# Performance work log

Hardware: AMD Instinct MI355X
Metric: run time of the kernel (lower is better)

The kernel has to match this reference:

```python
import jax, jax.numpy as jnp
import numpy as np

B, S, D, H = 4, 2048, 1024, 16
HD = D // H
BITS = 8
LEVELS = 2 ** BITS - 1          # number of negative log2 levels
SCALING = 32.0 / 16.0           # lora alpha / rank for 8-bit adapter
NEG_INF = -1e9


def log_fake_quant(x, reduce_axes):
    """Per-channel log-domain fake quantization with straight-through estimator.
    Scale = per-channel max-abs; magnitudes snapped to power-of-two fractions of scale."""
    s = jnp.maximum(jnp.max(jnp.abs(x), axis=reduce_axes, keepdims=True), 1e-8)
    ratio = jnp.clip(jnp.abs(x) / s, 2.0 ** (-LEVELS), 1.0)
    e = jnp.round(jnp.log2(ratio))                      # in [-LEVELS, 0]
    q = jnp.sign(x) * s * jnp.exp2(e)
    return x + jax.lax.stop_gradient(q - x)             # STE


def cpt_linear(x, W, b, lA, lB):
    """CPTLinear: fake-quantized activation/weight GEMM + bias + LoRA on the fp input."""
    xq = log_fake_quant(x, tuple(range(x.ndim - 1)))     # per last-dim channel
    Wq = log_fake_quant(W, (1,))                         # per output row (channel_dim=0)
    out = xq @ Wq.T + b
    return out + (x @ lA @ lB) * SCALING


def setup_inputs() -> dict:
    key = jax.random.key(0)
    ks = jax.random.split(key, 8)
    causal = jnp.tril(jnp.ones((S, S), dtype=bool))
    mask = jnp.where(causal, 0.0, NEG_INF).astype(jnp.float32)[None, None]  # [1,1,S,S]
    return {
        "hidden_states": jax.random.normal(ks[0], (B, S, D), jnp.float32),
        "attention_mask": mask,
        "W_attn": jax.random.normal(ks[1], (3 * D, D), jnp.float32) * 0.02,
        "b_attn": jnp.zeros((3 * D,), jnp.float32),
        "lA_attn": jax.random.normal(ks[2], (D, 16), jnp.float32) * 0.01,
        "lB_attn": jax.random.normal(ks[3], (16, 3 * D), jnp.float32) * 0.01,
        "W_proj": jax.random.normal(ks[4], (D, D), jnp.float32) * 0.02,
        "b_proj": jnp.zeros((D,), jnp.float32),
        "lA_proj": jax.random.normal(ks[5], (D, 16), jnp.float32) * 0.01,
        "lB_proj": jax.random.normal(ks[6], (16, D), jnp.float32) * 0.01,
    }


def reference(hidden_states, attention_mask, W_attn, b_attn, lA_attn, lB_attn,
              W_proj, b_proj, lA_proj, lB_proj):
    qkv = cpt_linear(hidden_states, W_attn, b_attn, lA_attn, lB_attn)  # [B,S,3D]
    q, k, v = jnp.split(qkv, 3, axis=-1)

    def to_heads(t):
        return t.reshape(B, S, H, HD).transpose(0, 2, 1, 3)            # [B,H,S,HD]

    q, k, v = to_heads(q), to_heads(k), to_heads(v)
    scores = jnp.einsum("bhqd,bhkd->bhqk", q, k) / np.float32(np.sqrt(HD))
    scores = scores + attention_mask
    attn = jax.nn.softmax(scores, axis=-1)                             # dropout: eval mode (identity)
    out = jnp.einsum("bhqk,bhkd->bhqd", attn, v)
    out = out.transpose(0, 2, 1, 3).reshape(B, S, D)
    return cpt_linear(out, W_proj, b_proj, lA_proj, lB_proj)
```

## Files before the change

kernel.cpp:

```cpp
#include <hip/hip_runtime.h>

#define SS 2048
#define DD 1024
#define DQKV 3072
#define KP 1088
#define NT64 17
#define MTOT 8192
#define QKSZ ((size_t)MTOT * DD)
#define SCL 0.18033688011112042f

typedef unsigned short us;
typedef __attribute__((ext_vector_type(8))) short bf16x8;
typedef __attribute__((ext_vector_type(4))) float f32x4;
typedef __attribute__((ext_vector_type(4))) unsigned u32x4;

#define WAITVM(N) asm volatile("s_waitcnt vmcnt(" #N ")" ::: "memory")
#define WAITLGKM0 asm volatile("s_waitcnt lgkmcnt(0)" ::: "memory")

__device__ __forceinline__ us f2bf(float f) {
    unsigned u = __float_as_uint(f);
    return (us)((u + 0x7fffu + ((u >> 16) & 1u)) >> 16);
}
__device__ __forceinline__ float bf2f(us h) { return __uint_as_float(((unsigned)h) << 16); }
__device__ __forceinline__ void split2(float q, us& h, us& l) {
    h = f2bf(q); l = f2bf(q - bf2f(h));
}
__device__ __forceinline__ unsigned cvtpk(float lo, float hi) {
    unsigned r;
    asm("v_cvt_pk_bf16_f32 %0, %1, %2" : "=v"(r) : "v"(lo), "v"(hi));
    return r;
}

__device__ __forceinline__ int logq_e(float ax, float s) {
    int e = 0;
    if (ax < s) {
        double r = (double)ax / (double)s;
        int ex;
        double mant = frexp(r, &ex);
        e = (mant >= 0.70710678118654752440) ? ex : ex - 1;
        e = (e < -255) ? -255 : e;
    }
    return e;
}
__device__ __forceinline__ float logq_exact(float x, float s) {
    float ax = fabsf(x);
    if (ax == 0.f) return copysignf(0.f, x);
    return copysignf(ldexpf(s, logq_e(ax, s)), x);
}

__device__ __forceinline__ void gll16(const void* g, void* l) {
    __builtin_amdgcn_global_load_lds(
        (const __attribute__((address_space(1))) void*)g,
        (__attribute__((address_space(3))) void*)l, 16, 0, 0);
}


__global__ void k_zero(unsigned* p, int n) {
    int i = blockIdx.x * 256 + threadIdx.x;
    if (i < n) p[i] = 0u;
}

__global__ void k_colmax(const float* __restrict__ x, unsigned* __restrict__ smax) {
    int c = blockIdx.x * 256 + threadIdx.x;
    int r0 = blockIdx.y * 128;
    float m = 0.f;
    for (int r = 0; r < 128; ++r) m = fmaxf(m, fabsf(x[(size_t)(r0 + r) * DD + c]));
    atomicMax(smax + c, __float_as_uint(m));
}

__global__ __launch_bounds__(256) void k_quant_lora(const float* __restrict__ x,
                                                    const unsigned* __restrict__ smax,
                                                    const float* __restrict__ lA,
                                                    us* __restrict__ xq) {
    __shared__ float red[4][16];
    int m = blockIdx.x, tx = threadIdx.x;
    int lane = tx & 63, w = tx >> 6;
    float4 xv = ((const float4*)(x + (size_t)m * DD))[tx];
    int c = tx * 4;
    float vv[4] = {xv.x, xv.y, xv.z, xv.w};
    ushort4 qh;
    us* ph = (us*)&qh;
#pragma unroll
    for (int j = 0; j < 4; ++j) {
        float s = fmaxf(__uint_as_float(smax[c + j]), 1e-8f);
        float sh = bf2f(f2bf(s));
        float ax = fabsf(vv[j]);
        if (ax == 0.f) ph[j] = (us)((__float_as_uint(vv[j]) >> 16) & 0x8000u);
        else ph[j] = f2bf(copysignf(ldexpf(sh, logq_e(ax, s)), vv[j]));
    }
    *(ushort4*)(xq + (size_t)m * KP + c) = qh;
    float acc[16];
#pragma unroll
    for (int r = 0; r < 16; ++r) acc[r] = 0.f;
#pragma unroll
    for (int j = 0; j < 4; ++j) {
        float xs = vv[j];
        const float4* lr = (const float4*)(lA + (size_t)(c + j) * 16);
        float4 a0 = lr[0], a1 = lr[1], a2 = lr[2], a3 = lr[3];
        acc[0] += xs * a0.x; acc[1] += xs * a0.y; acc[2] += xs * a0.z; acc[3] += xs * a0.w;
        acc[4] += xs * a1.x; acc[5] += xs * a1.y; acc[6] += xs * a1.z; acc[7] += xs * a1.w;
        acc[8] += xs * a2.x; acc[9] += xs * a2.y; acc[10] += xs * a2.z; acc[11] += xs * a2.w;
        acc[12] += xs * a3.x; acc[13] += xs * a3.y; acc[14] += xs * a3.z; acc[15] += xs * a3.w;
    }
#pragma unroll
    for (int msk = 1; msk < 64; msk <<= 1)
#pragma unroll
        for (int r = 0; r < 16; ++r) acc[r] += __shfl_xor(acc[r], msk);
    if (lane == 0)
#pragma unroll
        for (int r = 0; r < 16; ++r) red[w][r] = acc[r];
    __syncthreads();
    if (tx < 16) {
        float v = 2.0f * (red[0][tx] + red[1][tx] + red[2][tx] + red[3][tx]);
        us h, l; split2(v, h, l);
        xq[(size_t)m * KP + 1024 + tx] = h;
        xq[(size_t)m * KP + 1040 + tx] = l;
    } else if (tx == 16) {
        xq[(size_t)m * KP + 1056] = 0x3F80;
    } else if (tx < 48) {
        xq[(size_t)m * KP + 1040 + tx] = 0;
    }
}

__global__ __launch_bounds__(256) void k_quant_w(const float* __restrict__ W, const float* __restrict__ lB,
                                                 const float* __restrict__ bias,
                                                 const unsigned* __restrict__ smax,
                                                 us* __restrict__ wh, us* __restrict__ wl, int Nn) {
    __shared__ float red[4];
    int n = blockIdx.x, tx = threadIdx.x;
    int lane = tx & 63, w = tx >> 6;
    float4 wv = ((const float4*)(W + (size_t)n * DD))[tx];
    float m4 = fmaxf(fmaxf(fabsf(wv.x), fabsf(wv.y)), fmaxf(fabsf(wv.z), fabsf(wv.w)));
#pragma unroll
    for (int msk = 1; msk < 64; msk <<= 1) m4 = fmaxf(m4, __shfl_xor(m4, msk));
    if (lane == 0) red[w] = m4;
    __syncthreads();
    float t = fmaxf(fmaxf(fmaxf(red[0], red[1]), fmaxf(red[2], red[3])), 1e-8f);
    float vv[4] = {wv.x, wv.y, wv.z, wv.w};
    int c = tx * 4;
    ushort4 qh, ql;
    us* ph = (us*)&qh; us* pl = (us*)&ql;
#pragma unroll
    for (int j = 0; j < 4; ++j) {
        float s = fmaxf(__uint_as_float(smax[c + j]), 1e-8f);
        float sh = bf2f(f2bf(s));
        float rho = (s - sh) / sh;
        float q = logq_exact(vv[j], t);
        float wp = q + q * rho;
        split2(wp, ph[j], pl[j]);
    }
    *(ushort4*)(wh + (size_t)n * KP + c) = qh;
    *(ushort4*)(wl + (size_t)n * KP + c) = ql;
    if (tx < 64) {
        us h = 0, l = 0;
        if (tx < 32) { int r = tx & 15; split2(lB[(size_t)r * Nn + n], h, l); }
        else if (tx == 32) split2(bias[n], h, l);
        wh[(size_t)n * KP + 1024 + tx] = h;
        wl[(size_t)n * KP + 1024 + tx] = l;
    }
}


template <int MODE>
__global__ __launch_bounds__(512, 2) void k_gemm(const us* __restrict__ Aq_,
                                                 const us* __restrict__ Bh_, const us* __restrict__ Bl_,
                                                 float* __restrict__ C, int Nn,
                                                 us* __restrict__ Khg, us* __restrict__ Klg,
                                                 float* __restrict__ vbuf) {
    __shared__ us LA[2][16384];
    __shared__ us LBh[2][8192];
    __shared__ us LBl[2][8192];
    int tid = threadIdx.x;
    int bm = blockIdx.x, bn = blockIdx.y;
    int lane = tid & 63, w = tid >> 6;
    int wm = w >> 2, wn = w & 3;
    int l15 = lane & 15, l4 = lane >> 4;
    int srow = tid >> 3;
    int gsrc = ((tid & 7) ^ (srow & 7)) * 8;
    const us* aP  = Aq_ + (size_t)(bm * 256 + srow) * KP + gsrc;
    const us* bhP = Bh_ + (size_t)(bn * 128 + srow) * KP + gsrc;
    const us* blP = Bl_ + (size_t)(bn * 128 + srow) * KP + gsrc;
    f32x4 zero4 = {0.f, 0.f, 0.f, 0.f};
    f32x4 acc[8][2];
#pragma unroll
    for (int i = 0; i < 8; ++i) { acc[i][0] = zero4; acc[i][1] = zero4; }

#define GSTAGE(buf, kt)                                               \
    do {                                                              \
        int k0_ = (kt) * 64;                                          \
        gll16(aP + k0_,                    &LA[(buf)][0]     + tid * 8); \
        gll16(aP + (size_t)64  * KP + k0_, &LA[(buf)][4096]  + tid * 8); \
        gll16(aP + (size_t)128 * KP + k0_, &LA[(buf)][8192]  + tid * 8); \
        gll16(aP + (size_t)192 * KP + k0_, &LA[(buf)][12288] + tid * 8); \
        gll16(bhP + k0_,                   &LBh[(buf)][0]    + tid * 8); \
        gll16(bhP + (size_t)64 * KP + k0_, &LBh[(buf)][4096] + tid * 8); \
        gll16(blP + k0_,                   &LBl[(buf)][0]    + tid * 8); \
        gll16(blP + (size_t)64 * KP + k0_, &LBl[(buf)][4096] + tid * 8); \
    } while (0)

    GSTAGE(0, 0);
    GSTAGE(1, 1);
    WAITVM(8);
    __builtin_amdgcn_s_barrier();
    __builtin_amdgcn_sched_barrier(0);

    int gsw0 = ((l4)     ^ (l15 & 7)) * 8;
    int gsw1 = ((4 + l4) ^ (l15 & 7)) * 8;
    int cur = 0;
    for (int kt = 0; kt < NT64; ++kt) {
        const us* A0  = &LA[cur][0];
        const us* Bh0 = &LBh[cur][0];
        const us* Bl0 = &LBl[cur][0];
        bf16x8 a0[8], b0h[2], b0l[2];
#pragma unroll
        for (int i = 0; i < 8; ++i)
            a0[i] = *(const bf16x8*)(A0 + (wm * 128 + i * 16 + l15) * 64 + gsw0);
#pragma unroll
        for (int i = 0; i < 2; ++i) {
            b0h[i] = *(const bf16x8*)(Bh0 + (wn * 32 + i * 16 + l15) * 64 + gsw0);
            b0l[i] = *(const bf16x8*)(Bl0 + (wn * 32 + i * 16 + l15) * 64 + gsw0);
        }
        __builtin_amdgcn_s_setprio(1);
#pragma unroll
        for (int mi = 0; mi < 8; ++mi)
#pragma unroll
            for (int ni = 0; ni < 2; ++ni) {
                acc[mi][ni] = __builtin_amdgcn_mfma_f32_16x16x32_bf16(a0[mi], b0h[ni], acc[mi][ni], 0, 0, 0);
                acc[mi][ni] = __builtin_amdgcn_mfma_f32_16x16x32_bf16(a0[mi], b0l[ni], acc[mi][ni], 0, 0, 0);
            }
        __builtin_amdgcn_s_setprio(0);
        bf16x8 a1[8], b1h[2], b1l[2];
#pragma unroll
        for (int i = 0; i < 8; ++i)
            a1[i] = *(const bf16x8*)(A0 + (wm * 128 + i * 16 + l15) * 64 + gsw1);
#pragma unroll
        for (int i = 0; i < 2; ++i) {
            b1h[i] = *(const bf16x8*)(Bh0 + (wn * 32 + i * 16 + l15) * 64 + gsw1);
            b1l[i] = *(const bf16x8*)(Bl0 + (wn * 32 + i * 16 + l15) * 64 + gsw1);
        }
        WAITLGKM0;
        __builtin_amdgcn_sched_barrier(0);
        __builtin_amdgcn_s_barrier();
        __builtin_amdgcn_sched_barrier(0);
        if (kt + 2 < NT64) GSTAGE(cur, kt + 2);
        __builtin_amdgcn_s_setprio(1);
#pragma unroll
        for (int mi = 0; mi < 8; ++mi)
#pragma unroll
            for (int ni = 0; ni < 2; ++ni) {
                acc[mi][ni] = __builtin_amdgcn_mfma_f32_16x16x32_bf16(a1[mi], b1h[ni], acc[mi][ni], 0, 0, 0);
                acc[mi][ni] = __builtin_amdgcn_mfma_f32_16x16x32_bf16(a1[mi], b1l[ni], acc[mi][ni], 0, 0, 0);
            }
        __builtin_amdgcn_s_setprio(0);
        if (kt + 2 < NT64) { WAITVM(8); } else { WAITVM(0); }
        __builtin_amdgcn_s_barrier();
        __builtin_amdgcn_sched_barrier(0);
        cur ^= 1;
    }
#undef GSTAGE

    int plane = bn >> 3;
#pragma unroll
    for (int mi = 0; mi < 8; ++mi) {
#pragma unroll
        for (int ni = 0; ni < 2; ++ni) {
            int ncol = bn * 128 + wn * 32 + ni * 16 + l15;
            size_t mbase = (size_t)bm * 256 + wm * 128 + mi * 16 + l4 * 4;
#pragma unroll
            for (int rr = 0; rr < 4; ++rr) {
                float v = acc[mi][ni][rr];
                size_t m = mbase + rr;
                if (MODE == 0) {
                    C[m * (size_t)Nn + ncol] = v;
                } else {
                    int cc = ncol & 1023;
                    if (plane == 0) {
                        C[m * DD + cc] = v;
                    } else if (plane == 2) {
                        vbuf[m * DD + cc] = v;
                    } else {
                        us hh, ll; split2(v * SCL, hh, ll);
                        size_t d = ((size_t)((m >> 11) * 16 + (cc >> 6)) * SS + (m & 2047)) * 64 + (cc & 63);
                        Khg[d] = hh; Klg[d] = ll;
                    }
                }
            }
        }
    }
}


__global__ __launch_bounds__(256) void k_transpose_v(const float* __restrict__ vbuf,
                                                     us* __restrict__ vth, us* __restrict__ vtl) {
    __shared__ us th[64][72], tl[64][72];
    int st = blockIdx.x, bh = blockIdx.y;
    int bb = bh >> 4, h = bh & 15;
    int s0 = st * 64, tid = threadIdx.x;
    int sl = tid >> 2, c0 = (tid & 3) * 16;
    const float* src = vbuf + (size_t)(bb * SS + s0 + sl) * DD + h * 64 + c0;
#pragma unroll
    for (int j4 = 0; j4 < 4; ++j4) {
        float4 v = *(const float4*)(src + j4 * 4);
        float vv[4] = {v.x, v.y, v.z, v.w};
#pragma unroll
        for (int j = 0; j < 4; ++j) {
            us hh, ll; split2(vv[j], hh, ll);
            th[c0 + j4 * 4 + j][sl] = hh;
            tl[c0 + j4 * 4 + j][sl] = ll;
        }
    }
    __syncthreads();
#pragma unroll
    for (int p = 0; p < 2; ++p) {
        int gidx = p * 256 + tid;
        int hd = gidx >> 3, g = gidx & 7;
        int base = (g >> 2) * 32 + (g & 3) * 4;
        ushort4 a, b2, c, d2;
        a.x = th[hd][base];      a.y = th[hd][base + 1];  a.z = th[hd][base + 2];  a.w = th[hd][base + 3];
        b2.x = th[hd][base + 16]; b2.y = th[hd][base + 17]; b2.z = th[hd][base + 18]; b2.w = th[hd][base + 19];
        c.x = tl[hd][base];      c.y = tl[hd][base + 1];  c.z = tl[hd][base + 2];  c.w = tl[hd][base + 3];
        d2.x = tl[hd][base + 16]; d2.y = tl[hd][base + 17]; d2.z = tl[hd][base + 18]; d2.w = tl[hd][base + 19];
        size_t dof = ((size_t)bh * 64 + hd) * SS + s0 + g * 8;
        *(ushort4*)(vth + dof) = a;  *(ushort4*)(vth + dof + 4) = b2;
        *(ushort4*)(vtl + dof) = c;  *(ushort4*)(vtl + dof + 4) = d2;
    }
}


__constant__ int QPERM[8] = {7, 5, 3, 1, 0, 2, 4, 6};

__global__ __launch_bounds__(512, 2) void k_attn(float* qo,
                                                 const us* __restrict__ Khg, const us* __restrict__ Klg,
                                                 const us* __restrict__ vth, const us* __restrict__ vtl) {
    __shared__ us L[2][16384];
    int bh = blockIdx.x;
    int qt = QPERM[blockIdx.y];
    int b = bh >> 4, h = bh & 15;
    int q0 = qt * 256;
    int tid = threadIdx.x, w = tid >> 6, lane = tid & 63;
    int l15 = lane & 15, l4 = lane >> 4;
    int qw = q0 + w * 32;
    int swz = l15 & 7;

    bf16x8 qh[2][2], ql[2][2];
#pragma unroll
    for (int qb = 0; qb < 2; ++qb)
#pragma unroll
        for (int hf = 0; hf < 2; ++hf) {
            const float* qp = qo + (size_t)(b * SS + qw + qb * 16 + l15) * DD + h * 64 + hf * 32 + l4 * 8;
            float4 a = *(const float4*)qp;
            float4 c = *(const float4*)(qp + 4);
            float vv[8] = {a.x, a.y, a.z, a.w, c.x, c.y, c.z, c.w};
            bf16x8 hq, lq;
#pragma unroll
            for (int j = 0; j < 8; ++j) {
                us hh = f2bf(vv[j]);
                hq[j] = (short)hh;
                lq[j] = (short)f2bf(vv[j] - bf2f(hh));
            }
            qh[qb][hf] = hq; ql[qb][hf] = lq;
        }

    f32x4 zero4 = {0.f, 0.f, 0.f, 0.f};
    f32x4 of[2][4];
#pragma unroll
    for (int i = 0; i < 2; ++i)
#pragma unroll
        for (int j = 0; j < 4; ++j) of[i][j] = zero4;
    float mrow[2] = {-1e30f, -1e30f}, lrowp[2] = {0.f, 0.f};

    int r0 = tid >> 3, sl0 = (tid & 7) ^ (r0 & 7);
    int koff0 = (bh * SS + r0) * 64 + sl0 * 8;
    int voff0 = (bh * 64 + r0) * SS + sl0 * 8;

    int ntiles = qt * 4 + 4;

#define STAGE(buf, tt)                                           \
    do {                                                         \
        int kv_ = (tt) * 64;                                     \
        us* D_ = &L[(buf)][0];                                   \
        int kadd_ = kv_ << 6;                                    \
        gll16(Khg + koff0 + kadd_, D_ + tid * 8);                \
        gll16(Klg + koff0 + kadd_, D_ + 4096 + tid * 8);         \
        gll16(vth + voff0 + kv_, D_ + 8192 + tid * 8);           \
        gll16(vtl + voff0 + kv_, D_ + 12288 + tid * 8);          \
    } while (0)

    STAGE(0, 0);
    STAGE(1, 1);
    int cur = 0;

    for (int t = 0; t < ntiles; ++t) {
        int kv0 = t * 64;
        if (t + 1 < ntiles) WAITVM(4); else WAITVM(0);
        __builtin_amdgcn_s_barrier();

        if (kv0 <= qw + 31) {
            const us* Lc = &L[cur][0];

            f32x4 sf[4][2];
#pragma unroll
            for (int i = 0; i < 4; ++i) { sf[i][0] = zero4; sf[i][1] = zero4; }
            __builtin_amdgcn_s_setprio(1);
#pragma unroll
            for (int kb = 0; kb < 4; ++kb) {
                int rbase = (kb * 16 + l15) * 64;
#pragma unroll
                for (int hf = 0; hf < 2; ++hf) {
                    int off = rbase + (((hf * 4 + l4) ^ swz) * 8);
                    bf16x8 kh = *(const bf16x8*)(Lc + off);
                    bf16x8 kl = *(const bf16x8*)(Lc + 4096 + off);
#pragma unroll
                    for (int qb = 0; qb < 2; ++qb) {
                        sf[kb][qb] = __builtin_amdgcn_mfma_f32_16x16x32_bf16(kh, qh[qb][hf], sf[kb][qb], 0, 0, 0);
                        sf[kb][qb] = __builtin_amdgcn_mfma_f32_16x16x32_bf16(kh, ql[qb][hf], sf[kb][qb], 0, 0, 0);
                        sf[kb][qb] = __builtin_amdgcn_mfma_f32_16x16x32_bf16(kl, qh[qb][hf], sf[kb][qb], 0, 0, 0);
                    }
                }
            }
            __builtin_amdgcn_s_setprio(0);

            bool diag = (kv0 + 63 > qw);
            u32x4 PH[2][2], PL[2][2];
#pragma unroll
            for (int qb = 0; qb < 2; ++qb) {
                float pv[16];
                if (diag) {
                    int qg = qw + qb * 16 + l15;
#pragma unroll
                    for (int kb = 0; kb < 4; ++kb)
#pragma unroll
                        for (int rr = 0; rr < 4; ++rr) {
                            int kvg = kv0 + kb * 16 + l4 * 4 + rr;
                            pv[kb * 4 + rr] = (kvg > qg) ? -1e30f : sf[kb][qb][rr];
                        }
                } else {
#pragma unroll
                    for (int kb = 0; kb < 4; ++kb)
#pragma unroll
                        for (int rr = 0; rr < 4; ++rr)
                            pv[kb * 4 + rr] = sf[kb][qb][rr];
                }
                float t0 = fmaxf(fmaxf(pv[0], pv[1]), pv[2]);
                float t1 = fmaxf(fmaxf(pv[3], pv[4]), pv[5]);
                float t2 = fmaxf(fmaxf(pv[6], pv[7]), pv[8]);
                float t3 = fmaxf(fmaxf(pv[9], pv[10]), pv[11]);
                float t4 = fmaxf(fmaxf(pv[12], pv[13]), pv[14]);
                float tmax = fmaxf(fmaxf(fmaxf(t0, t1), fmaxf(t2, t3)), fmaxf(t4, pv[15]));
                tmax = fmaxf(tmax, __shfl_xor(tmax, 16));
                tmax = fmaxf(tmax, __shfl_xor(tmax, 32));
                float mcur = mrow[qb];
                if (!__all(tmax <= mcur + 8.0f)) {
                    float mnew = fmaxf(mcur, tmax);
                    float fac = __builtin_amdgcn_exp2f(mcur - mnew);
                    mrow[qb] = mnew; mcur = mnew;
                    lrowp[qb] *= fac;
                    float fr0 = __shfl(fac, l4 * 4 + 0);
                    float fr1 = __shfl(fac, l4 * 4 + 1);
                    float fr2 = __shfl(fac, l4 * 4 + 2);
                    float fr3 = __shfl(fac, l4 * 4 + 3);
#pragma unroll
                    for (int hb = 0; hb < 4; ++hb) {
                        of[qb][hb][0] *= fr0; of[qb][hb][1] *= fr1;
                        of[qb][hb][2] *= fr2; of[qb][hb][3] *= fr3;
                    }
                }
                float ps = 0.f;
#pragma unroll
                for (int i = 0; i < 16; ++i) {
                    pv[i] = __builtin_amdgcn_exp2f(pv[i] - mcur);
                    ps += pv[i];
                }
                lrowp[qb] += ps;
#pragma unroll
                for (int ks = 0; ks < 2; ++ks)
#pragma unroll
                    for (int c2 = 0; c2 < 4; ++c2) {
                        float p0 = pv[ks * 8 + c2 * 2], p1 = pv[ks * 8 + c2 * 2 + 1];
                        unsigned u = cvtpk(p0, p1);
                        float h0 = __uint_as_float(u << 16);
                        float h1 = __uint_as_float(u & 0xffff0000u);
                        unsigned ul = cvtpk(p0 - h0, p1 - h1);
                        PH[qb][ks][c2] = u; PL[qb][ks][c2] = ul;
                    }
            }

            __builtin_amdgcn_s_setprio(1);
#pragma unroll
            for (int hb = 0; hb < 4; ++hb) {
                int rbase = (hb * 16 + l15) * 64;
#pragma unroll
                for (int ks = 0; ks < 2; ++ks) {
                    int off = rbase + (((ks * 4 + l4) ^ swz) * 8);
                    bf16x8 vh = *(const bf16x8*)(Lc + 8192 + off);
                    bf16x8 vl = *(const bf16x8*)(Lc + 12288 + off);
#pragma unroll
                    for (int qb = 0; qb < 2; ++qb) {
                        bf16x8 pa = (bf16x8)PH[qb][ks];
                        bf16x8 pb = (bf16x8)PL[qb][ks];
                        of[qb][hb] = __builtin_amdgcn_mfma_f32_16x16x32_bf16(pa, vh, of[qb][hb], 0, 0, 0);
                        of[qb][hb] = __builtin_amdgcn_mfma_f32_16x16x32_bf16(pa, vl, of[qb][hb], 0, 0, 0);
                        of[qb][hb] = __builtin_amdgcn_mfma_f32_16x16x32_bf16(pb, vh, of[qb][hb], 0, 0, 0);
                    }
                }
            }
            __builtin_amdgcn_s_setprio(0);
        }

        __builtin_amdgcn_s_barrier();
        if (t + 2 < ntiles) STAGE(cur, t + 2);
        cur ^= 1;
    }
#undef STAGE

#pragma unroll
    for (int qb = 0; qb < 2; ++qb) {
        float lr = lrowp[qb];
        lr += __shfl_xor(lr, 16);
        lr += __shfl_xor(lr, 32);
        float linv = 1.f / lr;
        float f0 = __shfl(linv, l4 * 4 + 0);
        float f1 = __shfl(linv, l4 * 4 + 1);
        float f2 = __shfl(linv, l4 * 4 + 2);
        float f3 = __shfl(linv, l4 * 4 + 3);
        int qgb = qw + qb * 16 + l4 * 4;
#pragma unroll
        for (int hb = 0; hb < 4; ++hb) {
            int col = h * 64 + hb * 16 + l15;
            qo[((size_t)(b * SS + qgb + 0)) * DD + col] = of[qb][hb][0] * f0;
            qo[((size_t)(b * SS + qgb + 1)) * DD + col] = of[qb][hb][1] * f1;
            qo[((size_t)(b * SS + qgb + 2)) * DD + col] = of[qb][hb][2] * f2;
            qo[((size_t)(b * SS + qgb + 3)) * DD + col] = of[qb][hb][3] * f3;
        }
    }
}


extern "C" void kernel_launch(void* const* d_in, const int* in_sizes, int n_in,
                              void* d_out, int out_size, void* d_ws, size_t ws_size,
                              hipStream_t stream) {
    const float* hidden  = (const float*)d_in[0];
    const float* W_attn  = (const float*)d_in[2];
    const float* b_attn  = (const float*)d_in[3];
    const float* lA_attn = (const float*)d_in[4];
    const float* lB_attn = (const float*)d_in[5];
    const float* W_proj  = (const float*)d_in[6];
    const float* b_proj  = (const float*)d_in[7];
    const float* lA_proj = (const float*)d_in[8];
    const float* lB_proj = (const float*)d_in[9];
    float* out = (float*)d_out;

    char* ws = (char*)d_ws;
    unsigned* s1 = (unsigned*)(ws);
    unsigned* s2 = (unsigned*)(ws + 4096);
    us* xq  = (us*)(ws + 8192);
    us* vth = xq;
    us* wh1 = (us*)(ws + 8192 + 17825792);
    us* wl1 = (us*)(ws + 8192 + 17825792 + 6684672);
    us* wh2 = (us*)(ws + 8192 + 17825792 + 2 * 6684672);
    us* wl2 = (us*)(ws + 8192 + 17825792 + 2 * 6684672 + 2228224);
    char* pbase = ws + 8192 + 17825792 + 2 * 6684672 + 2 * 2228224;
    float* qbuf = (float*)pbase;
    float* vbuf = (float*)(pbase + 33554432);
    us* Khg = (us*)(pbase + 2 * (size_t)33554432);
    us* Klg = (us*)(pbase + 2 * (size_t)33554432 + 16777216);
    us* vtl = (us*)(pbase + 2 * (size_t)33554432 + 2 * (size_t)16777216);

    k_zero<<<8, 256, 0, stream>>>(s1, 2048);

    k_colmax<<<dim3(4, 64), 256, 0, stream>>>(hidden, s1);
    k_quant_lora<<<MTOT, 256, 0, stream>>>(hidden, s1, lA_attn, xq);
    k_quant_w<<<3072, 256, 0, stream>>>(W_attn, lB_attn, b_attn, s1, wh1, wl1, 3072);
    k_gemm<1><<<dim3(32, 24), 512, 0, stream>>>(xq, wh1, wl1, qbuf, DQKV, Khg, Klg, vbuf);

    k_transpose_v<<<dim3(32, 64), 256, 0, stream>>>(vbuf, vth, vtl);
    k_attn<<<dim3(64, 8), 512, 0, stream>>>(qbuf, Khg, Klg, vth, vtl);

    k_colmax<<<dim3(4, 64), 256, 0, stream>>>(qbuf, s2);
    k_quant_lora<<<MTOT, 256, 0, stream>>>(qbuf, s2, lA_proj, xq);
    k_quant_w<<<1024, 256, 0, stream>>>(W_proj, lB_proj, b_proj, s2, wh2, wl2, 1024);
    k_gemm<0><<<dim3(32, 8), 512, 0, stream>>>(xq, wh2, wl2, out, DD, nullptr, nullptr, nullptr);
}
```

Before: 494.1 us.

## Halve attention query tile to 128 rows per block and double grid

The attention kernel now gives each block 128 query rows (16 per wave) instead of 256 (32 per wave), and the grid grows from 8 to 16 query tiles per head. Query tiles are scheduled heaviest-first in simple reverse order, replacing the fixed permutation table. This is meant to raise block count and occupancy and to improve load balance across the causal triangle. In exchange, each K/V tile loaded into LDS is reused by half as many query rows, so total K/V traffic roughly doubles.

Result: faster. 447.4 us (median of 3 runs) (-9.5%).

```diff
diff --git a/kernel.cpp b/kernel.cpp
--- a/kernel.cpp
+++ b/kernel.cpp
@@ -327,53 +327,47 @@
 }
 
 
-__constant__ int QPERM[8] = {7, 5, 3, 1, 0, 2, 4, 6};
-
 __global__ __launch_bounds__(512, 2) void k_attn(float* qo,
                                                  const us* __restrict__ Khg, const us* __restrict__ Klg,
                                                  const us* __restrict__ vth, const us* __restrict__ vtl) {
     __shared__ us L[2][16384];
     int bh = blockIdx.x;
-    int qt = QPERM[blockIdx.y];
+    int qt = (int)(gridDim.y - 1) - blockIdx.y;
     int b = bh >> 4, h = bh & 15;
-    int q0 = qt * 256;
+    int q0 = qt * 128;
     int tid = threadIdx.x, w = tid >> 6, lane = tid & 63;
     int l15 = lane & 15, l4 = lane >> 4;
-    int qw = q0 + w * 32;
+    int qw = q0 + w * 16;
     int swz = l15 & 7;
 
-    bf16x8 qh[2][2], ql[2][2];
-#pragma unroll
-    for (int qb = 0; qb < 2; ++qb)
-#pragma unroll
-        for (int hf = 0; hf < 2; ++hf) {
-            const float* qp = qo + (size_t)(b * SS + qw + qb * 16 + l15) * DD + h * 64 + hf * 32 + l4 * 8;
-            float4 a = *(const float4*)qp;
-            float4 c = *(const float4*)(qp + 4);
-            float vv[8] = {a.x, a.y, a.z, a.w, c.x, c.y, c.z, c.w};
-            bf16x8 hq, lq;
-#pragma unroll
-            for (int j = 0; j < 8; ++j) {
-                us hh = f2bf(vv[j]);
-                hq[j] = (short)hh;
-                lq[j] = (short)f2bf(vv[j] - bf2f(hh));
-            }
-            qh[qb][hf] = hq; ql[qb][hf] = lq;
-        }
+    bf16x8 qh[2], ql[2];
+#pragma unroll
+    for (int hf = 0; hf < 2; ++hf) {
+        const float* qp = qo + (size_t)(b * SS + qw + l15) * DD + h * 64 + hf * 32 + l4 * 8;
+        float4 a = *(const float4*)qp;
+        float4 c = *(const float4*)(qp + 4);
+        float vv[8] = {a.x, a.y, a.z, a.w, c.x, c.y, c.z, c.w};
+        bf16x8 hq, lq;
+#pragma unroll
+        for (int j = 0; j < 8; ++j) {
+            us hh = f2bf(vv[j]);
+            hq[j] = (short)hh;
+            lq[j] = (short)f2bf(vv[j] - bf2f(hh));
+        }
+        qh[hf] = hq; ql[hf] = lq;
+    }
 
     f32x4 zero4 = {0.f, 0.f, 0.f, 0.f};
-    f32x4 of[2][4];
-#pragma unroll
-    for (int i = 0; i < 2; ++i)
-#pragma unroll
-        for (int j = 0; j < 4; ++j) of[i][j] = zero4;
-    float mrow[2] = {-1e30f, -1e30f}, lrowp[2] = {0.f, 0.f};
+    f32x4 of[4];
+#pragma unroll
+    for (int j = 0; j < 4; ++j) of[j] = zero4;
+    float mrow = -1e30f, lrowp = 0.f;
 
     int r0 = tid >> 3, sl0 = (tid & 7) ^ (r0 & 7);
     int koff0 = (bh * SS + r0) * 64 + sl0 * 8;
     int voff0 = (bh * 64 + r0) * SS + sl0 * 8;
 
-    int ntiles = qt * 4 + 4;
+    int ntiles = qt * 2 + 2;
 
 #define STAGE(buf, tt)                                           \
     do {                                                         \
@@ -395,12 +389,12 @@
         if (t + 1 < ntiles) WAITVM(4); else WAITVM(0);
         __builtin_amdgcn_s_barrier();
 
-        if (kv0 <= qw + 31) {
+        if (kv0 <= qw + 15) {
             const us* Lc = &L[cur][0];
 
-            f32x4 sf[4][2];
-#pragma unroll
-            for (int i = 0; i < 4; ++i) { sf[i][0] = zero4; sf[i][1] = zero4; }
+            f32x4 sf[4];
+#pragma unroll
+            for (int i = 0; i < 4; ++i) sf[i] = zero4;
             __builtin_amdgcn_s_setprio(1);
 #pragma unroll
             for (int kb = 0; kb < 4; ++kb) {
@@ -410,36 +404,32 @@
                     int off = rbase + (((hf * 4 + l4) ^ swz) * 8);
                     bf16x8 kh = *(const bf16x8*)(Lc + off);
                     bf16x8 kl = *(const bf16x8*)(Lc + 4096 + off);
-#pragma unroll
-                    for (int qb = 0; qb < 2; ++qb) {
-                        sf[kb][qb] = __builtin_amdgcn_mfma_f32_16x16x32_bf16(kh, qh[qb][hf], sf[kb][qb], 0, 0, 0);
-                        sf[kb][qb] = __builtin_amdgcn_mfma_f32_16x16x32_bf16(kh, ql[qb][hf], sf[kb][qb], 0, 0, 0);
-                        sf[kb][qb] = __builtin_amdgcn_mfma_f32_16x16x32_bf16(kl, qh[qb][hf], sf[kb][qb], 0, 0, 0);
-                    }
+                    sf[kb] = __builtin_amdgcn_mfma_f32_16x16x32_bf16(kh, qh[hf], sf[kb], 0, 0, 0);
+                    sf[kb] = __builtin_amdgcn_mfma_f32_16x16x32_bf16(kh, ql[hf], sf[kb], 0, 0, 0);
+                    sf[kb] = __builtin_amdgcn_mfma_f32_16x16x32_bf16(kl, qh[hf], sf[kb], 0, 0, 0);
                 }
             }
             __builtin_amdgcn_s_setprio(0);
 
             bool diag = (kv0 + 63 > qw);
-            u32x4 PH[2][2], PL[2][2];
-#pragma unroll
-            for (int qb = 0; qb < 2; ++qb) {
+            u32x4 PH[2], PL[2];
+            {
                 float pv[16];
                 if (diag) {
-                    int qg = qw + qb * 16 + l15;
+                    int qg = qw + l15;
 #pragma unroll
                     for (int kb = 0; kb < 4; ++kb)
 #pragma unroll
                         for (int rr = 0; rr < 4; ++rr) {
                             int kvg = kv0 + kb * 16 + l4 * 4 + rr;
-                            pv[kb * 4 + rr] = (kvg > qg) ? -1e30f : sf[kb][qb][rr];
+                            pv[kb * 4 + rr] = (kvg > qg) ? -1e30f : sf[kb][rr];
                         }
                 } else {
 #pragma unroll
                     for (int kb = 0; kb < 4; ++kb)
 #pragma unroll
                         for (int rr = 0; rr < 4; ++rr)
-                            pv[kb * 4 + rr] = sf[kb][qb][rr];
+                            pv[kb * 4 + rr] = sf[kb][rr];
                 }
                 float t0 = fmaxf(fmaxf(pv[0], pv[1]), pv[2]);
                 float t1 = fmaxf(fmaxf(pv[3], pv[4]), pv[5]);
@@ -449,20 +439,20 @@
                 float tmax = fmaxf(fmaxf(fmaxf(t0, t1), fmaxf(t2, t3)), fmaxf(t4, pv[15]));
                 tmax = fmaxf(tmax, __shfl_xor(tmax, 16));
                 tmax = fmaxf(tmax, __shfl_xor(tmax, 32));
-                float mcur = mrow[qb];
+                float mcur = mrow;
                 if (!__all(tmax <= mcur + 8.0f)) {
                     float mnew = fmaxf(mcur, tmax);
                     float fac = __builtin_amdgcn_exp2f(mcur - mnew);
-                    mrow[qb] = mnew; mcur = mnew;
-                    lrowp[qb] *= fac;
+                    mrow = mnew; mcur = mnew;
+                    lrowp *= fac;
                     float fr0 = __shfl(fac, l4 * 4 + 0);
                     float fr1 = __shfl(fac, l4 * 4 + 1);
                     float fr2 = __shfl(fac, l4 * 4 + 2);
                     float fr3 = __shfl(fac, l4 * 4 + 3);
 #pragma unroll
                     for (int hb = 0; hb < 4; ++hb) {
-                        of[qb][hb][0] *= fr0; of[qb][hb][1] *= fr1;
-                        of[qb][hb][2] *= fr2; of[qb][hb][3] *= fr3;
+                        of[hb][0] *= fr0; of[hb][1] *= fr1;
+                        of[hb][2] *= fr2; of[hb][3] *= fr3;
                     }
                 }
                 float ps = 0.f;
@@ -471,7 +461,7 @@
                     pv[i] = __builtin_amdgcn_exp2f(pv[i] - mcur);
                     ps += pv[i];
                 }
-                lrowp[qb] += ps;
+                lrowp += ps;
 #pragma unroll
                 for (int ks = 0; ks < 2; ++ks)
 #pragma unroll
@@ -481,7 +471,7 @@
                         float h0 = __uint_as_float(u << 16);
                         float h1 = __uint_as_float(u & 0xffff0000u);
                         unsigned ul = cvtpk(p0 - h0, p1 - h1);
-                        PH[qb][ks][c2] = u; PL[qb][ks][c2] = ul;
+                        PH[ks][c2] = u; PL[ks][c2] = ul;
                     }
             }
 
@@ -494,14 +484,11 @@
                     int off = rbase + (((ks * 4 + l4) ^ swz) * 8);
                     bf16x8 vh = *(const bf16x8*)(Lc + 8192 + off);
                     bf16x8 vl = *(const bf16x8*)(Lc + 12288 + off);
-#pragma unroll
-                    for (int qb = 0; qb < 2; ++qb) {
-                        bf16x8 pa = (bf16x8)PH[qb][ks];
-                        bf16x8 pb = (bf16x8)PL[qb][ks];
-                        of[qb][hb] = __builtin_amdgcn_mfma_f32_16x16x32_bf16(pa, vh, of[qb][hb], 0, 0, 0);
-                        of[qb][hb] = __builtin_amdgcn_mfma_f32_16x16x32_bf16(pa, vl, of[qb][hb], 0, 0, 0);
-                        of[qb][hb] = __builtin_amdgcn_mfma_f32_16x16x32_bf16(pb, vh, of[qb][hb], 0, 0, 0);
-                    }
+                    bf16x8 pa = (bf16x8)PH[ks];
+                    bf16x8 pb = (bf16x8)PL[ks];
+                    of[hb] = __builtin_amdgcn_mfma_f32_16x16x32_bf16(pa, vh, of[hb], 0, 0, 0);
+                    of[hb] = __builtin_amdgcn_mfma_f32_16x16x32_bf16(pa, vl, of[hb], 0, 0, 0);
+                    of[hb] = __builtin_amdgcn_mfma_f32_16x16x32_bf16(pb, vh, of[hb], 0, 0, 0);
                 }
             }
             __builtin_amdgcn_s_setprio(0);
@@ -513,9 +500,8 @@
     }
 #undef STAGE
 
-#pragma unroll
-    for (int qb = 0; qb < 2; ++qb) {
-        float lr = lrowp[qb];
+    {
+        float lr = lrowp;
         lr += __shfl_xor(lr, 16);
         lr += __shfl_xor(lr, 32);
         float linv = 1.f / lr;
@@ -523,14 +509,14 @@
         float f1 = __shfl(linv, l4 * 4 + 1);
         float f2 = __shfl(linv, l4 * 4 + 2);
         float f3 = __shfl(linv, l4 * 4 + 3);
-        int qgb = qw + qb * 16 + l4 * 4;
+        int qgb = qw + l4 * 4;
 #pragma unroll
         for (int hb = 0; hb < 4; ++hb) {
             int col = h * 64 + hb * 16 + l15;
-            qo[((size_t)(b * SS + qgb + 0)) * DD + col] = of[qb][hb][0] * f0;
-            qo[((size_t)(b * SS + qgb + 1)) * DD + col] = of[qb][hb][1] * f1;
-            qo[((size_t)(b * SS + qgb + 2)) * DD + col] = of[qb][hb][2] * f2;
-            qo[((size_t)(b * SS + qgb + 3)) * DD + col] = of[qb][hb][3] * f3;
+            qo[((size_t)(b * SS + qgb + 0)) * DD + col] = of[hb][0] * f0;
+            qo[((size_t)(b * SS + qgb + 1)) * DD + col] = of[hb][1] * f1;
+            qo[((size_t)(b * SS + qgb + 2)) * DD + col] = of[hb][2] * f2;
+            qo[((size_t)(b * SS + qgb + 3)) * DD + col] = of[hb][3] * f3;
         }
     }
 }
@@ -574,7 +560,7 @@
     k_gemm<1><<<dim3(32, 24), 512, 0, stream>>>(xq, wh1, wl1, qbuf, DQKV, Khg, Klg, vbuf);
 
     k_transpose_v<<<dim3(32, 64), 256, 0, stream>>>(vbuf, vth, vtl);
-    k_attn<<<dim3(64, 8), 512, 0, stream>>>(qbuf, Khg, Klg, vth, vtl);
+    k_attn<<<dim3(64, 16), 512, 0, stream>>>(qbuf, Khg, Klg, vth, vtl);
 
     k_colmax<<<dim3(4, 64), 256, 0, stream>>>(qbuf, s2);
     k_quant_lora<<<MTOT, 256, 0, stream>>>(qbuf, s2, lA_proj, xq);
```
